# Optimization experiments

Hardware: AMD Instinct MI355X
Metric: run time of the kernel (lower is better)

## Reference

```python
import jax, jax.numpy as jnp
import numpy as np

D_MODEL = 128
EXPAND = 8
D_INNER = EXPAND * D_MODEL            # 1024
HEADDIM = D_MODEL                     # headdim = int(in_channels*8/8)
NHEADS = D_INNER // HEADDIM           # 8
D_STATE = 128
D_CONV = 4
CONV_DIM = D_INNER + 2 * D_STATE      # 1280
D_IN_PROJ = 2 * D_INNER + 2 * D_STATE + NHEADS  # 2312
EPS = 1e-5
B_SZ, SEQ = 2, 2048


def setup_inputs() -> dict:
    key = jax.random.key(0)
    ks = jax.random.split(key, 16)
    n = jax.random.normal
    dt_init = jax.random.uniform(ks[4], (NHEADS,), minval=0.001, maxval=0.1)
    return dict(
        hidden_states=n(ks[0], (B_SZ, SEQ, D_MODEL), jnp.float32),
        w_in=n(ks[1], (D_IN_PROJ, D_MODEL), jnp.float32) / np.float32(np.sqrt(D_MODEL)),
        conv_w=n(ks[2], (CONV_DIM, D_CONV), jnp.float32) / np.float32(np.sqrt(D_CONV)),
        conv_b=n(ks[3], (CONV_DIM,), jnp.float32) * 0.01,
        dt_bias=jnp.log(jnp.expm1(dt_init)),  # inverse-softplus init (official)
        A_log=jnp.log(jax.random.uniform(ks[5], (NHEADS,), minval=1.0, maxval=16.0)),
        D_skip=jnp.ones((NHEADS,), jnp.float32),
        gnorm_w=jnp.ones((D_INNER,), jnp.float32),
        w_out=n(ks[6], (D_MODEL, D_INNER), jnp.float32) / np.float32(np.sqrt(D_INNER)),
        ln1_w=jnp.ones((D_MODEL,), jnp.float32),
        ln1_b=jnp.zeros((D_MODEL,), jnp.float32),
        ln2_w=jnp.ones((D_MODEL,), jnp.float32),
        ln2_b=jnp.zeros((D_MODEL,), jnp.float32),
        mlp_w=n(ks[7], (D_MODEL, D_MODEL), jnp.float32) / np.float32(np.sqrt(D_MODEL)),
        mlp_b=jnp.zeros((D_MODEL,), jnp.float32),
    )


def _layer_norm(x, w, b):
    m = x.mean(-1, keepdims=True)
    xc = x - m
    v = (xc * xc).mean(-1, keepdims=True)
    return xc * jax.lax.rsqrt(v + EPS) * w + b


def _mixer(u, w_in, conv_w, conv_b, dt_bias, A_log, D_skip, gnorm_w, w_out):
    b, l, _ = u.shape
    zxbcdt = u @ w_in.T                                    # (b,l,2312)
    z = zxbcdt[..., :D_INNER]                              # gate
    xBC = zxbcdt[..., D_INNER:D_INNER + CONV_DIM]
    dt = jax.nn.softplus(zxbcdt[..., -NHEADS:] + dt_bias)  # (b,l,h)
    # depthwise causal conv1d + SiLU
    xc = jnp.pad(xBC.swapaxes(1, 2), ((0, 0), (0, 0), (D_CONV - 1, 0)))
    xc = jax.lax.conv_general_dilated(xc, conv_w[:, None, :], (1,), 'VALID',
                                      feature_group_count=CONV_DIM)
    xBC = jax.nn.silu((xc + conv_b[None, :, None]).swapaxes(1, 2))
    x = xBC[..., :D_INNER].reshape(b, l, NHEADS, HEADDIM)  # (b,l,h,p)
    Bm = xBC[..., D_INNER:D_INNER + D_STATE]               # (b,l,n), ngroups=1
    Cm = xBC[..., D_INNER + D_STATE:]                      # (b,l,n)
    A = -jnp.exp(A_log)                                    # (h,)
    dA = jnp.exp(dt * A)                                   # (b,l,h)

    def step(S, inp):
        dA_t, dt_t, B_t, C_t, x_t = inp
        S = S * dA_t[:, :, None, None] + jnp.einsum('bh,bhp,bn->bhpn', dt_t, x_t, B_t)
        return S, jnp.einsum('bhpn,bn->bhp', S, C_t)

    S0 = jnp.zeros((b, NHEADS, HEADDIM, D_STATE), u.dtype)
    _, ys = jax.lax.scan(step, S0, (dA.swapaxes(0, 1), dt.swapaxes(0, 1),
                                    Bm.swapaxes(0, 1), Cm.swapaxes(0, 1),
                                    x.swapaxes(0, 1)))
    y = ys.swapaxes(0, 1) + D_skip[None, None, :, None] * x  # skip connection
    y = y.reshape(b, l, D_INNER) * jax.nn.silu(z)            # gated RMSNorm
    y = y * jax.lax.rsqrt((y * y).mean(-1, keepdims=True) + EPS) * gnorm_w
    return y @ w_out.T


def reference(hidden_states, w_in, conv_w, conv_b, dt_bias, A_log, D_skip,
              gnorm_w, w_out, ln1_w, ln1_b, ln2_w, ln2_b, mlp_w, mlp_b):
    residual = hidden_states
    h = _layer_norm(residual, ln1_w, ln1_b)
    h = _mixer(h, w_in, conv_w, conv_b, dt_bias, A_log, D_skip, gnorm_w, w_out)
    residual = h + residual
    h = _layer_norm(residual, ln2_w, ln2_b)
    return h @ mlp_w.T + mlp_b
```

## Files before the change

kernel.cpp:

```cpp
#include <hip/hip_runtime.h>
#include <hip/hip_bf16.h>

#define B_SZ 2
#define SEQ 2048
#define DMODEL 128
#define DINNER 1024
#define NHEADS 8
#define HEADDIM 128
#define DSTATE 128
#define CONVDIM 1280
#define NPROJ 2304
#define NTOK (B_SZ*SEQ)
#define CHUNK 64
#define NCHUNK (SEQ/CHUNK)
#define LDT 72

using bf16_t = __hip_bfloat16;
using short8 = __attribute__((ext_vector_type(8))) short;
using short4v= __attribute__((ext_vector_type(4))) short;
using f32x4  = __attribute__((ext_vector_type(4))) float;

__device__ __forceinline__ float silu_f(float x) { return x / (1.f + expf(-x)); }
__device__ __forceinline__ float bf2f(short s) {
    unsigned u = ((unsigned)(unsigned short)s) << 16;
    return __uint_as_float(u);
}
__device__ __forceinline__ short f2bf_s(float f) {
    bf16_t h = __float2bfloat16(f);
    return *(short*)&h;
}

__global__ __launch_bounds__(128) void head_fused(
        const float* __restrict__ hidden,
        const float* __restrict__ ln1_w, const float* __restrict__ ln1_b,
        const float* __restrict__ w_in,
        const float* __restrict__ dt_bias, const float* __restrict__ A_log,
        bf16_t* __restrict__ h_bf, float* __restrict__ dtb, float* __restrict__ ldAb,
        const float* __restrict__ wa, int na, const float* __restrict__ wb, int nb,
        const float* __restrict__ wc, int nc,
        bf16_t* __restrict__ oa, bf16_t* __restrict__ ob, bf16_t* __restrict__ oc) {
    int blk = blockIdx.x;
    if (blk >= NTOK) {
        int i = (blk - NTOK) * 128 + threadIdx.x;
        if (i < na) oa[i] = __float2bfloat16(wa[i]);
        else if (i < na + nb) ob[i - na] = __float2bfloat16(wb[i - na]);
        else if (i < na + nb + nc) oc[i - na - nb] = __float2bfloat16(wc[i - na - nb]);
        return;
    }
    int m = blk, t = threadIdx.x;
    __shared__ float red[128];
    __shared__ float sred[2][8];
    float v = hidden[(size_t)m*DMODEL + t];
    red[t] = v; __syncthreads();
    for (int s = 64; s > 0; s >>= 1) { if (t < s) red[t] += red[t+s]; __syncthreads(); }
    float mean = red[0] * (1.f/128.f);
    __syncthreads();
    float xc = v - mean;
    red[t] = xc * xc; __syncthreads();
    for (int s = 64; s > 0; s >>= 1) { if (t < s) red[t] += red[t+s]; __syncthreads(); }
    float var = red[0] * (1.f/128.f);
    float o = xc * rsqrtf(var + 1e-5f) * ln1_w[t] + ln1_b[t];
    h_bf[(size_t)m*DMODEL + t] = __float2bfloat16(o);
    int wave = t >> 6, lane = t & 63;
#pragma unroll
    for (int hd = 0; hd < NHEADS; hd++) {
        float p = o * w_in[(size_t)(NPROJ + hd)*DMODEL + t];
#pragma unroll
        for (int d = 1; d < 64; d <<= 1) p += __shfl_xor(p, d, 64);
        if (lane == 0) sred[wave][hd] = p;
    }
    __syncthreads();
    if (t < NHEADS) {
        float s = sred[0][t] + sred[1][t] + dt_bias[t];
        float dtv = (s > 20.f) ? s : log1pf(expf(s));
        float Av = -expf(A_log[t]);
        dtb[m*NHEADS + t] = dtv;
        ldAb[m*NHEADS + t] = dtv * Av;
    }
}

__global__ __launch_bounds__(256) void gemm_bf(const bf16_t* __restrict__ A,
                                               const bf16_t* __restrict__ W,
                                               bf16_t* __restrict__ C,
                                               int M, int N, int K) {
    int tid = threadIdx.x;
    int wave = tid >> 6, lane = tid & 63;
    int m0 = blockIdx.x * 64 + wave * 16;
    int n0 = blockIdx.y * 64;
    int lr = lane & 15, quad = lane >> 4;
    f32x4 acc[4];
#pragma unroll
    for (int j = 0; j < 4; j++) acc[j] = (f32x4){0.f, 0.f, 0.f, 0.f};
    for (int k0 = 0; k0 < K; k0 += 32) {
        short8 a = *(const short8*)(A + (size_t)(m0 + lr)*K + k0 + quad*8);
#pragma unroll
        for (int j = 0; j < 4; j++) {
            short8 b = *(const short8*)(W + (size_t)(n0 + j*16 + lr)*K + k0 + quad*8);
            acc[j] = __builtin_amdgcn_mfma_f32_16x16x32_bf16(a, b, acc[j], 0, 0, 0);
        }
    }
#pragma unroll
    for (int j = 0; j < 4; j++)
#pragma unroll
        for (int r = 0; r < 4; r++) {
            int row = m0 + quad*4 + r;
            int col = n0 + j*16 + lr;
            C[(size_t)row*N + col] = __float2bfloat16(acc[j][r]);
        }
}

__global__ __launch_bounds__(256) void conv_silu(const bf16_t* __restrict__ zxb,
                                                 const float* __restrict__ conv_w,
                                                 const float* __restrict__ conv_b,
                                                 bf16_t* __restrict__ xBCb) {
    int idx = blockIdx.x * 256 + threadIdx.x;
    if (idx >= NTOK * CONVDIM / 4) return;
    int c4 = (idx % (CONVDIM/4)) * 4;
    int m  = idx / (CONVDIM/4);
    int b = m >> 11, l = m & (SEQ - 1);
    float acc[4];
    f32x4 wv[4];
#pragma unroll
    for (int j = 0; j < 4; j++) {
        acc[j] = conv_b[c4 + j];
        wv[j] = *(const f32x4*)(conv_w + (c4 + j)*4);
    }
#pragma unroll
    for (int k = 0; k < 4; k++) {
        int ll = l - 3 + k;
        if (ll >= 0) {
            short4v v = *(const short4v*)(zxb + (size_t)(b*SEQ + ll)*NPROJ + DINNER + c4);
#pragma unroll
            for (int j = 0; j < 4; j++) acc[j] += bf2f(v[j]) * wv[j][k];
        }
    }
    short4v res;
#pragma unroll
    for (int j = 0; j < 4; j++) res[j] = f2bf_s(silu_f(acc[j]));
    *(short4v*)(xBCb + (size_t)m*CONVDIM + c4) = res;
}

__global__ __launch_bounds__(512) void scanA_mfma(const bf16_t* __restrict__ xBCb,
                                                  const float* __restrict__ dt,
                                                  const float* __restrict__ ldA,
                                                  bf16_t* __restrict__ Sloc,
                                                  float* __restrict__ Pbuf) {
    int bid = blockIdx.x;
    int c = bid & 31, hd = (bid >> 5) & 7, b = bid >> 8;
    int t = threadIdx.x, wave = t >> 6, lane = t & 63;
    int lr = lane & 15, quad = lane >> 4;
    __shared__ bf16_t XT[128*LDT];
    __shared__ bf16_t BT[128*LDT];
    __shared__ float ws[CHUNK];
    int m0tok = b*SEQ + c*CHUNK;
    if (t < 64) {
        float L = ldA[(m0tok + t)*NHEADS + hd];
#pragma unroll
        for (int d = 1; d < 64; d <<= 1) {
            float u = __shfl_up(L, d, 64);
            if (lane >= d) L += u;
        }
        float Ltot = __shfl(L, 63, 64);
        ws[t] = expf(Ltot - L) * dt[(m0tok + t)*NHEADS + hd];
        if (t == 63) Pbuf[bid] = expf(Ltot);
    }
    __syncthreads();
#pragma unroll 4
    for (int i = 0; i < 16; i++) {
        int idx = i*512 + t;
        int tt = idx >> 7, p = idx & 127;
        const bf16_t* row = xBCb + (size_t)(m0tok + tt)*CONVDIM;
        float xv = bf2f(*(const short*)&row[hd*HEADDIM + p]);
        XT[p*LDT + tt] = __float2bfloat16(xv * ws[tt]);
        BT[p*LDT + tt] = row[DINNER + p];
    }
    __syncthreads();
    int m0w = wave * 16;
    f32x4 acc[8];
#pragma unroll
    for (int ni = 0; ni < 8; ni++) acc[ni] = (f32x4){0.f,0.f,0.f,0.f};
#pragma unroll
    for (int k0 = 0; k0 < 64; k0 += 32) {
        short8 a = *(const short8*)&XT[(m0w + lr)*LDT + k0 + quad*8];
#pragma unroll
        for (int ni = 0; ni < 8; ni++) {
            short8 bb = *(const short8*)&BT[(ni*16 + lr)*LDT + k0 + quad*8];
            acc[ni] = __builtin_amdgcn_mfma_f32_16x16x32_bf16(a, bb, acc[ni], 0, 0, 0);
        }
    }
    bf16_t* outp = Sloc + (size_t)bid * 16384;
#pragma unroll
    for (int ni = 0; ni < 8; ni++)
#pragma unroll
        for (int r = 0; r < 4; r++) {
            int p = m0w + quad*4 + r;
            int n = ni*16 + lr;
            outp[p*128 + n] = __float2bfloat16(acc[ni][r]);
        }
}

__global__ __launch_bounds__(256) void scanB(const bf16_t* __restrict__ Sloc,
                                             bf16_t* __restrict__ Sini,
                                             const float* __restrict__ Pbuf) {
    int bid = blockIdx.x;
    int bh = bid >> 5, slice = bid & 31;
    int t = threadIdx.x;
    int off = slice*512 + t*2;
    size_t base = (size_t)bh * NCHUNK * 16384;
    float run0 = 0.f, run1 = 0.f;
    for (int cc = 0; cc < NCHUNK; cc++) {
        unsigned raw = *(const unsigned*)(Sloc + base + (size_t)cc*16384 + off);
        float P = Pbuf[bh*NCHUNK + cc];
        unsigned o0 = (unsigned)(unsigned short)f2bf_s(run0);
        unsigned o1 = (unsigned)(unsigned short)f2bf_s(run1);
        *(unsigned*)(Sini + base + (size_t)cc*16384 + off) = o0 | (o1 << 16);
        run0 = run0*P + bf2f((short)(raw & 0xffff));
        run1 = run1*P + bf2f((short)(raw >> 16));
    }
}

__global__ __launch_bounds__(512) void scanC_mfma(const bf16_t* __restrict__ xBCb,
                                                  const float* __restrict__ dt,
                                                  const float* __restrict__ ldA,
                                                  const bf16_t* __restrict__ Sini,
                                                  const float* __restrict__ Dskip,
                                                  bf16_t* __restrict__ ybuf) {
    int bid = blockIdx.x;
    int c = bid & 31, hd = (bid >> 5) & 7, b = bid >> 8;
    int t = threadIdx.x, wave = t >> 6, lane = t & 63;
    int lr = lane & 15, quad = lane >> 4;
    __shared__ bf16_t XT[128*LDT];
    __shared__ bf16_t Mlds[64*LDT];
    __shared__ float Ls[CHUNK], dts[CHUNK];
    int m0tok = b*SEQ + c*CHUNK;
    if (t < 64) {
        float L = ldA[(m0tok + t)*NHEADS + hd];
#pragma unroll
        for (int d = 1; d < 64; d <<= 1) {
            float u = __shfl_up(L, d, 64);
            if (lane >= d) L += u;
        }
        Ls[t] = L;
        dts[t] = dt[(m0tok + t)*NHEADS + hd];
    }
#pragma unroll 4
    for (int i = 0; i < 16; i++) {
        int idx = i*512 + t;
        int tt = idx >> 7, p = idx & 127;
        XT[p*LDT + tt] = xBCb[(size_t)(m0tok + tt)*CONVDIM + hd*HEADDIM + p];
    }
    __syncthreads();
    const bf16_t* Crow = xBCb + (size_t)m0tok*CONVDIM + DINNER + DSTATE;
    const bf16_t* Brow = xBCb + (size_t)m0tok*CONVDIM + DINNER;
    {
        int trow0 = (wave & 3) * 16;
        int sh = wave >> 2;
        f32x4 g[2];
        g[0] = (f32x4){0.f,0.f,0.f,0.f}; g[1] = (f32x4){0.f,0.f,0.f,0.f};
#pragma unroll
        for (int k0 = 0; k0 < 128; k0 += 32) {
            short8 a = *(const short8*)(Crow + (size_t)(trow0 + lr)*CONVDIM + k0 + quad*8);
#pragma unroll
            for (int si = 0; si < 2; si++) {
                short8 bb = *(const short8*)(Brow + (size_t)(sh*32 + si*16 + lr)*CONVDIM + k0 + quad*8);
                g[si] = __builtin_amdgcn_mfma_f32_16x16x32_bf16(a, bb, g[si], 0, 0, 0);
            }
        }
#pragma unroll
        for (int si = 0; si < 2; si++)
#pragma unroll
            for (int r = 0; r < 4; r++) {
                int tt = trow0 + quad*4 + r;
                int ss = sh*32 + si*16 + lr;
                float v = (ss <= tt) ? g[si][r] * expf(Ls[tt] - Ls[ss]) * dts[ss] : 0.f;
                Mlds[tt*LDT + ss] = __float2bfloat16(v);
            }
    }
    __syncthreads();
    int p0 = wave * 16;
    f32x4 acc[4];
#pragma unroll
    for (int mi = 0; mi < 4; mi++) acc[mi] = (f32x4){0.f,0.f,0.f,0.f};
    const bf16_t* Sb = Sini + (size_t)bid * 16384;
#pragma unroll
    for (int k0 = 0; k0 < 128; k0 += 32) {
        short8 bb = *(const short8*)(Sb + (size_t)(p0 + lr)*128 + k0 + quad*8);
#pragma unroll
        for (int mi = 0; mi < 4; mi++) {
            short8 aC = *(const short8*)(Crow + (size_t)(mi*16 + lr)*CONVDIM + k0 + quad*8);
            acc[mi] = __builtin_amdgcn_mfma_f32_16x16x32_bf16(aC, bb, acc[mi], 0, 0, 0);
        }
    }
#pragma unroll
    for (int mi = 0; mi < 4; mi++) {
#pragma unroll
        for (int r = 0; r < 4; r++) acc[mi][r] *= expf(Ls[mi*16 + quad*4 + r]);
    }
#pragma unroll
    for (int k0 = 0; k0 < 64; k0 += 32) {
        short8 bb = *(const short8*)&XT[(p0 + lr)*LDT + k0 + quad*8];
#pragma unroll
        for (int mi = 0; mi < 4; mi++) {
            short8 aM = *(const short8*)&Mlds[(mi*16 + lr)*LDT + k0 + quad*8];
            acc[mi] = __builtin_amdgcn_mfma_f32_16x16x32_bf16(aM, bb, acc[mi], 0, 0, 0);
        }
    }
    float dsk = Dskip[hd];
#pragma unroll
    for (int mi = 0; mi < 4; mi++)
#pragma unroll
        for (int r = 0; r < 4; r++) {
            int tt = mi*16 + quad*4 + r;
            int pp = p0 + lr;
            float xv = bf2f(*(const short*)&XT[pp*LDT + tt]);
            int m = m0tok + tt;
            ybuf[(size_t)m*DINNER + hd*HEADDIM + pp] = __float2bfloat16(acc[mi][r] + dsk*xv);
        }
}

__global__ __launch_bounds__(512) void gate_out_mlp(const bf16_t* __restrict__ ybuf,
                                                    const bf16_t* __restrict__ zxb,
                                                    const float* __restrict__ gw,
                                                    const bf16_t* __restrict__ Wb,
                                                    const float* __restrict__ resid,
                                                    const float* __restrict__ w2,
                                                    const float* __restrict__ b2,
                                                    const bf16_t* __restrict__ Wm,
                                                    const float* __restrict__ mb,
                                                    float* __restrict__ out) {
    int blk = blockIdx.x, t = threadIdx.x;
    int tok0 = blk * 16;
    int tt = t >> 5, cg = t & 31;
    __shared__ bf16_t A1[16*1032];
    __shared__ float MIX[16*132];
    __shared__ bf16_t A2[16*136];
    {
        int ch0 = cg * 32;
        const bf16_t* yr = ybuf + (size_t)(tok0 + tt)*DINNER + ch0;
        const bf16_t* zr = zxb  + (size_t)(tok0 + tt)*NPROJ  + ch0;
        float vals[32];
        float ss = 0.f;
#pragma unroll
        for (int i = 0; i < 32; i += 4) {
            short4v y = *(const short4v*)(yr + i);
            short4v z = *(const short4v*)(zr + i);
#pragma unroll
            for (int r = 0; r < 4; r++) {
                float v = bf2f(y[r]) * silu_f(bf2f(z[r]));
                vals[i + r] = v; ss += v*v;
            }
        }
#pragma unroll
        for (int d = 1; d < 32; d <<= 1) ss += __shfl_xor(ss, d, 64);
        float rstd = rsqrtf(ss*(1.f/1024.f) + 1e-5f);
#pragma unroll
        for (int i = 0; i < 32; i += 4) {
            short4v pk;
#pragma unroll
            for (int r = 0; r < 4; r++) pk[r] = f2bf_s(vals[i+r]*rstd*gw[ch0+i+r]);
            *(short4v*)&A1[tt*1032 + ch0 + i] = pk;
        }
    }
    __syncthreads();
    int wave = t >> 6, lane = t & 63, lr = lane & 15, quad = lane >> 4;
    {
        f32x4 acc = (f32x4){0.f,0.f,0.f,0.f};
        int col = wave*16 + lr;
        for (int k0 = 0; k0 < 1024; k0 += 32) {
            short8 a = *(const short8*)&A1[lr*1032 + k0 + quad*8];
            short8 bb = *(const short8*)(Wb + (size_t)col*DINNER + k0 + quad*8);
            acc = __builtin_amdgcn_mfma_f32_16x16x32_bf16(a, bb, acc, 0, 0, 0);
        }
#pragma unroll
        for (int r = 0; r < 4; r++)
            MIX[(quad*4 + r)*132 + col] = acc[r];
    }
    __syncthreads();
    {
        int ch0 = cg * 4;
        const float* rr = resid + (size_t)(tok0 + tt)*DMODEL + ch0;
        float v[4];
        f32x4 r0 = *(const f32x4*)rr;
#pragma unroll
        for (int r = 0; r < 4; r++) v[r] = MIX[tt*132 + ch0 + r] + r0[r];
        float s = 0.f, sq = 0.f;
#pragma unroll
        for (int i = 0; i < 4; i++) { s += v[i]; sq += v[i]*v[i]; }
#pragma unroll
        for (int d = 1; d < 32; d <<= 1) { s += __shfl_xor(s, d, 64); sq += __shfl_xor(sq, d, 64); }
        float mean = s * (1.f/128.f);
        float var  = sq * (1.f/128.f) - mean*mean;
        float rstd = rsqrtf(var + 1e-5f);
        short4v pk;
#pragma unroll
        for (int r = 0; r < 4; r++)
            pk[r] = f2bf_s((v[r] - mean)*rstd*w2[ch0+r] + b2[ch0+r]);
        *(short4v*)&A2[tt*136 + ch0] = pk;
    }
    __syncthreads();
    {
        f32x4 acc = (f32x4){0.f,0.f,0.f,0.f};
        int col = wave*16 + lr;
#pragma unroll
        for (int k0 = 0; k0 < 128; k0 += 32) {
            short8 a = *(const short8*)&A2[lr*136 + k0 + quad*8];
            short8 bb = *(const short8*)(Wm + (size_t)col*DMODEL + k0 + quad*8);
            acc = __builtin_amdgcn_mfma_f32_16x16x32_bf16(a, bb, acc, 0, 0, 0);
        }
#pragma unroll
        for (int r = 0; r < 4; r++) {
            int row = tok0 + quad*4 + r;
            out[(size_t)row*DMODEL + col] = acc[r] + mb[col];
        }
    }
}

extern "C" void kernel_launch(void* const* d_in, const int* in_sizes, int n_in,
                              void* d_out, int out_size, void* d_ws, size_t ws_size,
                              hipStream_t stream) {
    const float* hidden  = (const float*)d_in[0];
    const float* w_in    = (const float*)d_in[1];
    const float* conv_w  = (const float*)d_in[2];
    const float* conv_b  = (const float*)d_in[3];
    const float* dt_bias = (const float*)d_in[4];
    const float* A_log   = (const float*)d_in[5];
    const float* D_skip  = (const float*)d_in[6];
    const float* gnorm_w = (const float*)d_in[7];
    const float* w_out   = (const float*)d_in[8];
    const float* ln1_w   = (const float*)d_in[9];
    const float* ln1_b   = (const float*)d_in[10];
    const float* ln2_w   = (const float*)d_in[11];
    const float* ln2_b   = (const float*)d_in[12];
    const float* mlp_w   = (const float*)d_in[13];
    const float* mlp_b   = (const float*)d_in[14];
    float* out = (float*)d_out;

    char* ws = (char*)d_ws;
    size_t off = 0;
    auto alloc = [&](size_t bytes) -> void* {
        void* p = ws + off;
        off = (off + bytes + 255) & ~(size_t)255;
        return p;
    };
    bf16_t* h_bf   = (bf16_t*)alloc((size_t)NTOK*DMODEL*2);
    bf16_t* w_in_bf= (bf16_t*)alloc((size_t)NPROJ*DMODEL*2);
    bf16_t* w_out_bf=(bf16_t*)alloc((size_t)DMODEL*DINNER*2);
    bf16_t* mlp_bf = (bf16_t*)alloc((size_t)DMODEL*DMODEL*2);
    bf16_t* zx_bf  = (bf16_t*)alloc((size_t)NTOK*NPROJ*2);
    bf16_t* xBCb   = (bf16_t*)alloc((size_t)NTOK*CONVDIM*2);
    float*  dtb    = (float*) alloc((size_t)NTOK*NHEADS*4);
    float*  ldAb   = (float*) alloc((size_t)NTOK*NHEADS*4);
    bf16_t* Sloc   = (bf16_t*)alloc((size_t)B_SZ*NHEADS*NCHUNK*16384*2);
    bf16_t* Sini   = (bf16_t*)alloc((size_t)B_SZ*NHEADS*NCHUNK*16384*2);
    float*  Pbuf   = (float*) alloc((size_t)B_SZ*NHEADS*NCHUNK*4);
    bf16_t* ybuf   = (bf16_t*)alloc((size_t)NTOK*DINNER*2);
    (void)ws_size; (void)in_sizes; (void)n_in; (void)out_size;

    {
        int na = NPROJ*DMODEL, nb = DMODEL*DINNER, nc = DMODEL*DMODEL;
        int castBlocks = (na + nb + nc + 127) / 128;
        head_fused<<<NTOK + castBlocks, 128, 0, stream>>>(
            hidden, ln1_w, ln1_b, w_in, dt_bias, A_log, h_bf, dtb, ldAb,
            w_in, na, w_out, nb, mlp_w, nc, w_in_bf, w_out_bf, mlp_bf);
    }
    gemm_bf<<<dim3(NTOK/64, NPROJ/64), 256, 0, stream>>>(h_bf, w_in_bf, zx_bf,
                                                         NTOK, NPROJ, DMODEL);
    conv_silu<<<((size_t)NTOK*CONVDIM/4 + 255)/256, 256, 0, stream>>>(zx_bf, conv_w, conv_b, xBCb);
    scanA_mfma<<<B_SZ*NHEADS*NCHUNK, 512, 0, stream>>>(xBCb, dtb, ldAb, Sloc, Pbuf);
    scanB<<<B_SZ*NHEADS*NCHUNK, 256, 0, stream>>>(Sloc, Sini, Pbuf);
    scanC_mfma<<<B_SZ*NHEADS*NCHUNK, 512, 0, stream>>>(xBCb, dtb, ldAb, Sini, D_skip, ybuf);
    gate_out_mlp<<<NTOK/16, 512, 0, stream>>>(ybuf, zx_bf, gnorm_w, w_out_bf,
                                              hidden, ln2_w, ln2_b, mlp_bf, mlp_b, out);
}
```

Measured before the change: 185.8 us.

## Fuse depthwise conv+SiLU into scan kernels and stage B/C in LDS

Removes the separate conv_silu kernel and its xBC intermediate buffer. scanA and scanC now compute the causal 4-tap convolution and SiLU on the fly from the projection output. scanC also stages the convolved B and C chunk tiles in shared memory instead of reading them from global memory for the MFMA operands. This saves one launch and a global write/read round trip, at the cost of redundant conv work across the 8 heads for B/C, strided scalar bf16 loads, and more LDS use per block.

```diff
diff --git a/kernel.cpp b/kernel.cpp
--- a/kernel.cpp
+++ b/kernel.cpp
@@ -14,6 +14,7 @@
 #define CHUNK 64
 #define NCHUNK (SEQ/CHUNK)
 #define LDT 72
+#define LDN 136
 
 using bf16_t = __hip_bfloat16;
 using short8 = __attribute__((ext_vector_type(8))) short;
@@ -109,38 +110,9 @@
         }
 }
 
-__global__ __launch_bounds__(256) void conv_silu(const bf16_t* __restrict__ zxb,
-                                                 const float* __restrict__ conv_w,
-                                                 const float* __restrict__ conv_b,
-                                                 bf16_t* __restrict__ xBCb) {
-    int idx = blockIdx.x * 256 + threadIdx.x;
-    if (idx >= NTOK * CONVDIM / 4) return;
-    int c4 = (idx % (CONVDIM/4)) * 4;
-    int m  = idx / (CONVDIM/4);
-    int b = m >> 11, l = m & (SEQ - 1);
-    float acc[4];
-    f32x4 wv[4];
-#pragma unroll
-    for (int j = 0; j < 4; j++) {
-        acc[j] = conv_b[c4 + j];
-        wv[j] = *(const f32x4*)(conv_w + (c4 + j)*4);
-    }
-#pragma unroll
-    for (int k = 0; k < 4; k++) {
-        int ll = l - 3 + k;
-        if (ll >= 0) {
-            short4v v = *(const short4v*)(zxb + (size_t)(b*SEQ + ll)*NPROJ + DINNER + c4);
-#pragma unroll
-            for (int j = 0; j < 4; j++) acc[j] += bf2f(v[j]) * wv[j][k];
-        }
-    }
-    short4v res;
-#pragma unroll
-    for (int j = 0; j < 4; j++) res[j] = f2bf_s(silu_f(acc[j]));
-    *(short4v*)(xBCb + (size_t)m*CONVDIM + c4) = res;
-}
-
-__global__ __launch_bounds__(512) void scanA_mfma(const bf16_t* __restrict__ xBCb,
+__global__ __launch_bounds__(512) void scanA_mfma(const bf16_t* __restrict__ zxb,
+                                                  const float* __restrict__ conv_w,
+                                                  const float* __restrict__ conv_b,
                                                   const float* __restrict__ dt,
                                                   const float* __restrict__ ldA,
                                                   bf16_t* __restrict__ Sloc,
@@ -153,6 +125,7 @@
     __shared__ bf16_t BT[128*LDT];
     __shared__ float ws[CHUNK];
     int m0tok = b*SEQ + c*CHUNK;
+    int l0 = c*CHUNK;
     if (t < 64) {
         float L = ldA[(m0tok + t)*NHEADS + hd];
 #pragma unroll
@@ -165,14 +138,26 @@
         if (t == 63) Pbuf[bid] = expf(Ltot);
     }
     __syncthreads();
-#pragma unroll 4
+#pragma unroll 2
     for (int i = 0; i < 16; i++) {
         int idx = i*512 + t;
         int tt = idx >> 7, p = idx & 127;
-        const bf16_t* row = xBCb + (size_t)(m0tok + tt)*CONVDIM;
-        float xv = bf2f(*(const short*)&row[hd*HEADDIM + p]);
-        XT[p*LDT + tt] = __float2bfloat16(xv * ws[tt]);
-        BT[p*LDT + tt] = row[DINNER + p];
+        int l = l0 + tt;
+        float accX = conv_b[hd*HEADDIM + p];
+        float accB = conv_b[1024 + p];
+        f32x4 wX = *(const f32x4*)(conv_w + (hd*HEADDIM + p)*4);
+        f32x4 wB = *(const f32x4*)(conv_w + (1024 + p)*4);
+#pragma unroll
+        for (int k = 0; k < 4; k++) {
+            int ll = l - 3 + k;
+            if (ll >= 0) {
+                const bf16_t* zrow = zxb + (size_t)(b*SEQ + ll)*NPROJ + DINNER;
+                accX += bf2f(*(const short*)&zrow[hd*HEADDIM + p]) * wX[k];
+                accB += bf2f(*(const short*)&zrow[1024 + p]) * wB[k];
+            }
+        }
+        XT[p*LDT + tt] = __float2bfloat16(silu_f(accX) * ws[tt]);
+        BT[p*LDT + tt] = __float2bfloat16(silu_f(accB));
     }
     __syncthreads();
     int m0w = wave * 16;
@@ -219,7 +204,9 @@
     }
 }
 
-__global__ __launch_bounds__(512) void scanC_mfma(const bf16_t* __restrict__ xBCb,
+__global__ __launch_bounds__(512) void scanC_mfma(const bf16_t* __restrict__ zxb,
+                                                  const float* __restrict__ conv_w,
+                                                  const float* __restrict__ conv_b,
                                                   const float* __restrict__ dt,
                                                   const float* __restrict__ ldA,
                                                   const bf16_t* __restrict__ Sini,
@@ -231,8 +218,11 @@
     int lr = lane & 15, quad = lane >> 4;
     __shared__ bf16_t XT[128*LDT];
     __shared__ bf16_t Mlds[64*LDT];
+    __shared__ bf16_t Ct[64*LDN];
+    __shared__ bf16_t Bt[64*LDN];
     __shared__ float Ls[CHUNK], dts[CHUNK];
     int m0tok = b*SEQ + c*CHUNK;
+    int l0 = c*CHUNK;
     if (t < 64) {
         float L = ldA[(m0tok + t)*NHEADS + hd];
 #pragma unroll
@@ -243,15 +233,32 @@
         Ls[t] = L;
         dts[t] = dt[(m0tok + t)*NHEADS + hd];
     }
-#pragma unroll 4
+#pragma unroll 2
     for (int i = 0; i < 16; i++) {
         int idx = i*512 + t;
         int tt = idx >> 7, p = idx & 127;
-        XT[p*LDT + tt] = xBCb[(size_t)(m0tok + tt)*CONVDIM + hd*HEADDIM + p];
-    }
-    __syncthreads();
-    const bf16_t* Crow = xBCb + (size_t)m0tok*CONVDIM + DINNER + DSTATE;
-    const bf16_t* Brow = xBCb + (size_t)m0tok*CONVDIM + DINNER;
+        int l = l0 + tt;
+        float accX = conv_b[hd*HEADDIM + p];
+        float accB = conv_b[1024 + p];
+        float accC = conv_b[1152 + p];
+        f32x4 wX = *(const f32x4*)(conv_w + (hd*HEADDIM + p)*4);
+        f32x4 wB = *(const f32x4*)(conv_w + (1024 + p)*4);
+        f32x4 wC = *(const f32x4*)(conv_w + (1152 + p)*4);
+#pragma unroll
+        for (int k = 0; k < 4; k++) {
+            int ll = l - 3 + k;
+            if (ll >= 0) {
+                const bf16_t* zrow = zxb + (size_t)(b*SEQ + ll)*NPROJ + DINNER;
+                accX += bf2f(*(const short*)&zrow[hd*HEADDIM + p]) * wX[k];
+                accB += bf2f(*(const short*)&zrow[1024 + p]) * wB[k];
+                accC += bf2f(*(const short*)&zrow[1152 + p]) * wC[k];
+            }
+        }
+        XT[p*LDT + tt] = __float2bfloat16(silu_f(accX));
+        Bt[tt*LDN + p] = __float2bfloat16(silu_f(accB));
+        Ct[tt*LDN + p] = __float2bfloat16(silu_f(accC));
+    }
+    __syncthreads();
     {
         int trow0 = (wave & 3) * 16;
         int sh = wave >> 2;
@@ -259,10 +266,10 @@
         g[0] = (f32x4){0.f,0.f,0.f,0.f}; g[1] = (f32x4){0.f,0.f,0.f,0.f};
 #pragma unroll
         for (int k0 = 0; k0 < 128; k0 += 32) {
-            short8 a = *(const short8*)(Crow + (size_t)(trow0 + lr)*CONVDIM + k0 + quad*8);
+            short8 a = *(const short8*)&Ct[(trow0 + lr)*LDN + k0 + quad*8];
 #pragma unroll
             for (int si = 0; si < 2; si++) {
-                short8 bb = *(const short8*)(Brow + (size_t)(sh*32 + si*16 + lr)*CONVDIM + k0 + quad*8);
+                short8 bb = *(const short8*)&Bt[(sh*32 + si*16 + lr)*LDN + k0 + quad*8];
                 g[si] = __builtin_amdgcn_mfma_f32_16x16x32_bf16(a, bb, g[si], 0, 0, 0);
             }
         }
@@ -287,7 +294,7 @@
         short8 bb = *(const short8*)(Sb + (size_t)(p0 + lr)*128 + k0 + quad*8);
 #pragma unroll
         for (int mi = 0; mi < 4; mi++) {
-            short8 aC = *(const short8*)(Crow + (size_t)(mi*16 + lr)*CONVDIM + k0 + quad*8);
+            short8 aC = *(const short8*)&Ct[(mi*16 + lr)*LDN + k0 + quad*8];
             acc[mi] = __builtin_amdgcn_mfma_f32_16x16x32_bf16(aC, bb, acc[mi], 0, 0, 0);
         }
     }
@@ -447,7 +454,6 @@
     bf16_t* w_out_bf=(bf16_t*)alloc((size_t)DMODEL*DINNER*2);
     bf16_t* mlp_bf = (bf16_t*)alloc((size_t)DMODEL*DMODEL*2);
     bf16_t* zx_bf  = (bf16_t*)alloc((size_t)NTOK*NPROJ*2);
-    bf16_t* xBCb   = (bf16_t*)alloc((size_t)NTOK*CONVDIM*2);
     float*  dtb    = (float*) alloc((size_t)NTOK*NHEADS*4);
     float*  ldAb   = (float*) alloc((size_t)NTOK*NHEADS*4);
     bf16_t* Sloc   = (bf16_t*)alloc((size_t)B_SZ*NHEADS*NCHUNK*16384*2);
@@ -465,10 +471,11 @@
     }
     gemm_bf<<<dim3(NTOK/64, NPROJ/64), 256, 0, stream>>>(h_bf, w_in_bf, zx_bf,
                                                          NTOK, NPROJ, DMODEL);
-    conv_silu<<<((size_t)NTOK*CONVDIM/4 + 255)/256, 256, 0, stream>>>(zx_bf, conv_w, conv_b, xBCb);
-    scanA_mfma<<<B_SZ*NHEADS*NCHUNK, 512, 0, stream>>>(xBCb, dtb, ldAb, Sloc, Pbuf);
+    scanA_mfma<<<B_SZ*NHEADS*NCHUNK, 512, 0, stream>>>(zx_bf, conv_w, conv_b, dtb, ldAb,
+                                                       Sloc, Pbuf);
     scanB<<<B_SZ*NHEADS*NCHUNK, 256, 0, stream>>>(Sloc, Sini, Pbuf);
-    scanC_mfma<<<B_SZ*NHEADS*NCHUNK, 512, 0, stream>>>(xBCb, dtb, ldAb, Sini, D_skip, ybuf);
+    scanC_mfma<<<B_SZ*NHEADS*NCHUNK, 512, 0, stream>>>(zx_bf, conv_w, conv_b, dtb, ldAb,
+                                                       Sini, D_skip, ybuf);
     gate_out_mlp<<<NTOK/16, 512, 0, stream>>>(ybuf, zx_bf, gnorm_w, w_out_bf,
                                               hidden, ln2_w, ln2_b, mlp_bf, mlp_b, out);
 }
```

Measured after the change: 187.6 us. No clear change (+1.0%).
